# Optimization experiments

Hardware: AMD Instinct MI355X
Metric: run time of the kernel (lower is better)

The kernel has to match this reference:

```python
import jax, jax.numpy as jnp
import numpy as np

N = 8192      # number of tokens (input_dim in the original code)
D = 512       # hidden/embedding dim
R = 20        # number of dependency labels (2R with reverses)
L = 2         # num_layers
OUT = 256     # output_dim


def setup_inputs() -> dict:
    key = jax.random.key(0)
    ks = jax.random.split(key, 10)
    s = 0.02
    return {
        "x": jax.random.normal(ks[0], (N, D), dtype=jnp.float32),
        "dep_idx": jax.random.randint(ks[1], (N,), 0, N, dtype=jnp.int32),
        "rel_idx": jax.random.randint(ks[2], (N,), 0, R, dtype=jnp.int32),
        "gov_idx": jax.random.randint(ks[3], (N,), 0, N, dtype=jnp.int32),
        "W_self": jax.random.normal(ks[4], (L, D, D), dtype=jnp.float32) * s,
        "b_self": jax.random.normal(ks[5], (L, D), dtype=jnp.float32) * s,
        "W_rel": jax.random.normal(ks[6], (L, 2 * R, D, D), dtype=jnp.float32) * s,
        "b_rel": jax.random.normal(ks[7], (L, 2 * R, D), dtype=jnp.float32) * s,
        "W_ff": jax.random.normal(ks[8], (OUT, D), dtype=jnp.float32) * s,
        "b_ff": jax.random.normal(ks[9], (OUT,), dtype=jnp.float32) * s,
    }


def _gcn_layer(x, dep_idx, rel_idx, gov_idx, Ws, bs, Wr, br):
    # self transform applied to every token: temp[idx] = W_self @ x[idx] + b
    out = x @ Ws.T + bs  # [N, D]
    # relation-specific message passing: loop over the small fixed label set.
    # For each relation r: transform ALL nodes once (dense GEMM), then
    # mask-gather-scatter only the edges carrying that relation.
    for r in range(R):
        m = (rel_idx == r)[:, None]                      # [E, 1]
        # forward direction: dependent += W_r @ x[governor] + b_r
        h_f = x @ Wr[r].T + br[r]                        # [N, D]
        out = out.at[dep_idx].add(jnp.where(m, h_f[gov_idx], 0.0))
        # reverse direction: governor += W_{r}_r @ x[dependent] + b
        h_b = x @ Wr[R + r].T + br[R + r]                # [N, D]
        out = out.at[gov_idx].add(jnp.where(m, h_b[dep_idx], 0.0))
    return jax.nn.relu(out)


def reference(x, dep_idx, rel_idx, gov_idx, W_self, b_self, W_rel, b_rel, W_ff, b_ff):
    h = x
    for l in range(L):  # dropout_rate=0.0 -> dropout is identity; last layer has no dropout anyway
        h = _gcn_layer(h, dep_idx, rel_idx, gov_idx, W_self[l], b_self[l], W_rel[l], b_rel[l])
    return h @ W_ff.T + b_ff  # [N, OUT]
```

## Files before the change

### kernel.cpp

```cpp
#include <hip/hip_runtime.h>

#define N_TOK 8192
#define DIM   512
#define NREL  20
#define NGRP  40
#define OUTD  256
#define MAXT  168
#define MAXP  (MAXT*128)

typedef unsigned short u16;
typedef u16    u16x8  __attribute__((ext_vector_type(8)));
typedef __bf16 bf16x8 __attribute__((ext_vector_type(8)));
typedef float  f32x4  __attribute__((ext_vector_type(4)));

__device__ __forceinline__ u16 f2bf(float f) {
  union { float f; unsigned u; } v; v.f = f;
  return (u16)((v.u + 0x7FFFu + ((v.u >> 16) & 1u)) >> 16);
}

__global__ void k_cvt(const float* __restrict__ in, u16* __restrict__ out,
                      int n4, int relu) {
  int stride = gridDim.x * blockDim.x;
  for (int i = blockIdx.x * blockDim.x + threadIdx.x; i < n4; i += stride) {
    float4 v = reinterpret_cast<const float4*>(in)[i];
    if (relu) {
      v.x = fmaxf(v.x, 0.f); v.y = fmaxf(v.y, 0.f);
      v.z = fmaxf(v.z, 0.f); v.w = fmaxf(v.w, 0.f);
    }
    reinterpret_cast<ushort4*>(out)[i] =
        make_ushort4(f2bf(v.x), f2bf(v.y), f2bf(v.z), f2bf(v.w));
  }
}

__global__ void k_hist(const int* __restrict__ rel, int* __restrict__ cnt) {
  int e = blockIdx.x * blockDim.x + threadIdx.x;
  if (e < N_TOK) atomicAdd(&cnt[rel[e]], 1);
}
__global__ void k_scan2(const int* __restrict__ cnt, int* __restrict__ po,
                        int* __restrict__ segtab) {
  if (threadIdx.x == 0) {
    int tile = 0, p = 0;
    for (int s = 0; s < NGRP; ++s) {
      int r = (s < NREL) ? s : s - NREL;
      po[s] = p;
      int nt = (cnt[r] + 127) >> 7;
      for (int i = 0; i < nt; ++i) segtab[tile++] = s;
      p += nt << 7;
    }
    po[NGRP] = p;
    for (; tile < MAXT; ++tile) segtab[tile] = -1;
  }
}
__global__ void k_fill2(const int* __restrict__ rel, const int* __restrict__ dep,
                        const int* __restrict__ gov, const int* __restrict__ po,
                        int* __restrict__ cur, int* __restrict__ msrc,
                        int* __restrict__ mdst) {
  int e = blockIdx.x * blockDim.x + threadIdx.x;
  if (e < N_TOK) {
    int r = rel[e];
    int p = atomicAdd(&cur[r], 1);
    int pf = po[r] + p, pb = po[NREL + r] + p;
    msrc[pf] = gov[e]; mdst[pf] = dep[e];
    msrc[pb] = dep[e]; mdst[pb] = gov[e];
  }
}

template <int KIND>
__global__ __launch_bounds__(256) void k_mm(
    const u16* __restrict__ A, const u16* __restrict__ Wb,
    const float* __restrict__ bias,
    const int* __restrict__ msrc, const int* __restrict__ mdst,
    const int* __restrict__ segtab,
    float* __restrict__ Cf, int Nn)
{
  int seg = 0;
  if (KIND == 1) { seg = segtab[blockIdx.x]; if (seg < 0) return; }
  const int m0 = blockIdx.x * 128, n0 = blockIdx.y * 128;
  const u16* Bsrc = Wb + (KIND == 1 ? (size_t)seg * DIM * DIM : 0);

  __shared__ u16 As[128 * 64];
  __shared__ u16 Bs[128 * 64];

  const int t = threadIdx.x, w = t >> 6, l = t & 63;
  const int wm = (w >> 1) * 64, wn = (w & 1) * 64;
  const int lc = l & 15, h8 = l >> 4;
  const int wch = (t & 7) ^ ((t >> 3) & 7);

  const u16* gApt[4]; const u16* gBpt[4]; bool azero[4];
#pragma unroll
  for (int p = 0; p < 4; ++p) {
    const int row = p * 32 + (t >> 3);
    int arow;
    if (KIND == 1) { arow = msrc[m0 + row]; azero[p] = (arow < 0); if (arow < 0) arow = 0; }
    else { arow = m0 + row; azero[p] = false; }
    gApt[p] = A + (size_t)arow * DIM + (t & 7) * 8;
    gBpt[p] = Bsrc + (size_t)(n0 + row) * DIM + (t & 7) * 8;
  }

  f32x4 acc[4][4] = {};

  for (int k0 = 0; k0 < DIM; k0 += 64) {
#pragma unroll
    for (int p = 0; p < 4; ++p) {
      const int row = p * 32 + (t >> 3);
      u16x8 av = {0, 0, 0, 0, 0, 0, 0, 0};
      if (KIND != 1 || !azero[p]) av = *reinterpret_cast<const u16x8*>(gApt[p] + k0);
      *reinterpret_cast<u16x8*>(&As[row * 64 + wch * 8]) = av;
      u16x8 bw = *reinterpret_cast<const u16x8*>(gBpt[p] + k0);
      *reinterpret_cast<u16x8*>(&Bs[row * 64 + wch * 8]) = bw;
    }
    __syncthreads();
#pragma unroll
    for (int ks = 0; ks < 2; ++ks) {
      const int rc = ks * 4 + h8;
      bf16x8 af[4], bfr[4];
#pragma unroll
      for (int mi = 0; mi < 4; ++mi)
        af[mi] = *reinterpret_cast<const bf16x8*>(&As[(wm + mi * 16 + lc) * 64 + (rc ^ (lc & 7)) * 8]);
#pragma unroll
      for (int ni = 0; ni < 4; ++ni)
        bfr[ni] = *reinterpret_cast<const bf16x8*>(&Bs[(wn + ni * 16 + lc) * 64 + (rc ^ (lc & 7)) * 8]);
#pragma unroll
      for (int mi = 0; mi < 4; ++mi)
#pragma unroll
        for (int ni = 0; ni < 4; ++ni)
          acc[mi][ni] = __builtin_amdgcn_mfma_f32_16x16x32_bf16(af[mi], bfr[ni], acc[mi][ni], 0, 0, 0);
    }
    __syncthreads();
  }

  float bv[4];
  const float* bb = (KIND == 1) ? (bias + (size_t)seg * DIM) : bias;
#pragma unroll
  for (int ni = 0; ni < 4; ++ni) bv[ni] = bb[n0 + wn + ni * 16 + lc];

#pragma unroll
  for (int mi = 0; mi < 4; ++mi)
#pragma unroll
    for (int j = 0; j < 4; ++j) {
      const int rloc = wm + mi * 16 + h8 * 4 + j;
      if (KIND == 1) {
        const int dst = mdst[m0 + rloc];
        if (dst >= 0) {
          float* pout = Cf + (size_t)dst * DIM + n0 + wn + lc;
#pragma unroll
          for (int ni = 0; ni < 4; ++ni)
            unsafeAtomicAdd(pout + ni * 16, acc[mi][ni][j] + bv[ni]);
        }
      } else {
        float* pout = Cf + (size_t)(m0 + rloc) * Nn + n0 + wn + lc;
#pragma unroll
        for (int ni = 0; ni < 4; ++ni)
          pout[ni * 16] = acc[mi][ni][j] + bv[ni];
      }
    }
}

extern "C" void kernel_launch(void* const* d_in, const int* in_sizes, int n_in,
                              void* d_out, int out_size, void* d_ws, size_t ws_size,
                              hipStream_t stream) {
  const float* x      = (const float*)d_in[0];
  const int*   dep    = (const int*)d_in[1];
  const int*   rel    = (const int*)d_in[2];
  const int*   gov    = (const int*)d_in[3];
  const float* W_self = (const float*)d_in[4];
  const float* b_self = (const float*)d_in[5];
  const float* W_rel  = (const float*)d_in[6];
  const float* b_rel  = (const float*)d_in[7];
  const float* W_ff   = (const float*)d_in[8];
  const float* b_ff   = (const float*)d_in[9];
  float* out = (float*)d_out;

  char* ws = (char*)d_ws;
  size_t o = 0;
  auto alloc = [&](size_t bytes) -> void* {
    void* p = ws + o;
    o = (o + bytes + 255) & ~(size_t)255;
    return p;
  };
  u16*   Wrel_bf  = (u16*)alloc((size_t)2 * NGRP * DIM * DIM * 2);
  u16*   Wself_bf = (u16*)alloc((size_t)2 * DIM * DIM * 2);
  u16*   Wff_bf   = (u16*)alloc((size_t)OUTD * DIM * 2);
  u16*   hb0      = (u16*)alloc((size_t)N_TOK * DIM * 2);
  u16*   hb1      = (u16*)alloc((size_t)N_TOK * DIM * 2);
  float* outf     = (float*)alloc((size_t)N_TOK * DIM * 4);
  int*   cnt      = (int*)alloc(NREL * 4);
  int*   po       = (int*)alloc((NGRP + 1) * 4);
  int*   cur      = (int*)alloc(NREL * 4);
  int*   msrc     = (int*)alloc(MAXP * 4);
  int*   mdst     = (int*)alloc(MAXP * 4);
  int*   segtab   = (int*)alloc(MAXT * 4);
  (void)ws_size; (void)in_sizes; (void)n_in; (void)out_size;

  k_cvt<<<2048, 256, 0, stream>>>(W_rel,  Wrel_bf,  2 * NGRP * DIM * DIM / 4, 0);
  k_cvt<<<512,  256, 0, stream>>>(W_self, Wself_bf, 2 * DIM * DIM / 4, 0);
  k_cvt<<<128,  256, 0, stream>>>(W_ff,   Wff_bf,   OUTD * DIM / 4, 0);
  k_cvt<<<2048, 256, 0, stream>>>(x, hb0, N_TOK * DIM / 4, 0);

  hipMemsetAsync(cnt, 0, NREL * 4, stream);
  hipMemsetAsync(cur, 0, NREL * 4, stream);
  hipMemsetAsync(msrc, 0xFF, MAXP * 4, stream);
  hipMemsetAsync(mdst, 0xFF, MAXP * 4, stream);
  k_hist<<<N_TOK / 256, 256, 0, stream>>>(rel, cnt);
  k_scan2<<<1, 64, 0, stream>>>(cnt, po, segtab);
  k_fill2<<<N_TOK / 256, 256, 0, stream>>>(rel, dep, gov, po, cur, msrc, mdst);

  u16* hin = hb0;
  u16* hout = hb1;
  for (int l = 0; l < 2; ++l) {
    k_mm<0><<<dim3(64, 4), 256, 0, stream>>>(
        hin, Wself_bf + (size_t)l * DIM * DIM, b_self + (size_t)l * DIM,
        nullptr, nullptr, nullptr, outf, DIM);
    k_mm<1><<<dim3(MAXT, 4), 256, 0, stream>>>(
        hin, Wrel_bf + (size_t)l * NGRP * DIM * DIM,
        b_rel + (size_t)l * NGRP * DIM, msrc, mdst, segtab, outf, DIM);
    k_cvt<<<2048, 256, 0, stream>>>(outf, hout, N_TOK * DIM / 4, 1);
    u16* tmp = hin; hin = hout; hout = tmp;
  }

  k_mm<0><<<dim3(64, 2), 256, 0, stream>>>(
      hin, Wff_bf, b_ff, nullptr, nullptr, nullptr, out, OUTD);
}
```

Before: 362.6 us.

## Merge self and relation GEMMs into one launch and fuse setup kernels

Combines the four weight/input conversion launches into one multi-segment kernel and replaces the histogram, scan and memset launches with a single-block prep kernel that builds offsets and the tile-to-segment table in shared memory. The self-transform GEMM and the relation scatter GEMM now share one launch with a combined grid. Self tiles also accumulate with atomics into an output buffer that is zeroed by a memset each layer. This cuts launch count and lets self and relation tiles run concurrently, at the cost of an extra memset and atomic writes for the dense part.

New measurement: 371.4 us. 2.4% more time.

```diff
diff --git a/kernel.cpp b/kernel.cpp
--- a/kernel.cpp
+++ b/kernel.cpp
@@ -5,6 +5,7 @@
 #define NREL  20
 #define NGRP  40
 #define OUTD  256
+#define STILE 64
 #define MAXT  168
 #define MAXP  (MAXT*128)
 
@@ -18,39 +19,63 @@
   return (u16)((v.u + 0x7FFFu + ((v.u >> 16) & 1u)) >> 16);
 }
 
-__global__ void k_cvt(const float* __restrict__ in, u16* __restrict__ out,
-                      int n4, int relu) {
-  int stride = gridDim.x * blockDim.x;
+__global__ void k_cvt4(const float* __restrict__ s0, u16* __restrict__ d0, int m0,
+                       const float* __restrict__ s1, u16* __restrict__ d1, int m1,
+                       const float* __restrict__ s2, u16* __restrict__ d2, int m2,
+                       const float* __restrict__ s3, u16* __restrict__ d3, int m3) {
+  const int stride = gridDim.x * blockDim.x;
+  const int t0 = blockIdx.x * blockDim.x + threadIdx.x;
+#define CVT_LOOP(S, D, N)                                                    \
+  for (int i = t0; i < N; i += stride) {                                     \
+    float4 v = reinterpret_cast<const float4*>(S)[i];                        \
+    reinterpret_cast<ushort4*>(D)[i] =                                       \
+        make_ushort4(f2bf(v.x), f2bf(v.y), f2bf(v.z), f2bf(v.w));            \
+  }
+  CVT_LOOP(s0, d0, m0) CVT_LOOP(s1, d1, m1) CVT_LOOP(s2, d2, m2) CVT_LOOP(s3, d3, m3)
+#undef CVT_LOOP
+}
+
+__global__ void k_cvtr(const float* __restrict__ in, u16* __restrict__ out, int n4) {
+  const int stride = gridDim.x * blockDim.x;
   for (int i = blockIdx.x * blockDim.x + threadIdx.x; i < n4; i += stride) {
     float4 v = reinterpret_cast<const float4*>(in)[i];
-    if (relu) {
-      v.x = fmaxf(v.x, 0.f); v.y = fmaxf(v.y, 0.f);
-      v.z = fmaxf(v.z, 0.f); v.w = fmaxf(v.w, 0.f);
-    }
     reinterpret_cast<ushort4*>(out)[i] =
-        make_ushort4(f2bf(v.x), f2bf(v.y), f2bf(v.z), f2bf(v.w));
-  }
-}
-
-__global__ void k_hist(const int* __restrict__ rel, int* __restrict__ cnt) {
-  int e = blockIdx.x * blockDim.x + threadIdx.x;
-  if (e < N_TOK) atomicAdd(&cnt[rel[e]], 1);
-}
-__global__ void k_scan2(const int* __restrict__ cnt, int* __restrict__ po,
-                        int* __restrict__ segtab) {
-  if (threadIdx.x == 0) {
-    int tile = 0, p = 0;
+        make_ushort4(f2bf(fmaxf(v.x, 0.f)), f2bf(fmaxf(v.y, 0.f)),
+                     f2bf(fmaxf(v.z, 0.f)), f2bf(fmaxf(v.w, 0.f)));
+  }
+}
+
+__global__ void k_prep(const int* __restrict__ rel, int* __restrict__ po,
+                       int* __restrict__ segtab, int* __restrict__ cur) {
+  __shared__ int hist[NREL];
+  __shared__ int tpo[NGRP + 1];
+  const int t = threadIdx.x;
+  if (t < NREL) { hist[t] = 0; cur[t] = 0; }
+  __syncthreads();
+  for (int e = t; e < N_TOK; e += 256) atomicAdd(&hist[rel[e]], 1);
+  __syncthreads();
+  if (t == 0) {
+    int acc = 0;
     for (int s = 0; s < NGRP; ++s) {
       int r = (s < NREL) ? s : s - NREL;
-      po[s] = p;
-      int nt = (cnt[r] + 127) >> 7;
-      for (int i = 0; i < nt; ++i) segtab[tile++] = s;
-      p += nt << 7;
-    }
-    po[NGRP] = p;
-    for (; tile < MAXT; ++tile) segtab[tile] = -1;
-  }
-}
+      tpo[s] = acc;
+      acc += (hist[r] + 127) >> 7;
+    }
+    tpo[NGRP] = acc;
+  }
+  __syncthreads();
+  if (t <= NGRP) po[t] = tpo[t] << 7;
+  if (t < MAXT) {
+    int s = -1;
+    if (t < tpo[NGRP]) {
+      int lo = 0, hi = NGRP - 1;
+      while (lo < hi) { int mid = (lo + hi + 1) >> 1; if (tpo[mid] <= t) lo = mid; else hi = mid - 1; }
+      s = lo;
+    }
+    segtab[t] = s;
+  }
+}
+
 __global__ void k_fill2(const int* __restrict__ rel, const int* __restrict__ dep,
                         const int* __restrict__ gov, const int* __restrict__ po,
                         int* __restrict__ cur, int* __restrict__ msrc,
@@ -67,16 +92,28 @@
 
 template <int KIND>
 __global__ __launch_bounds__(256) void k_mm(
-    const u16* __restrict__ A, const u16* __restrict__ Wb,
-    const float* __restrict__ bias,
+    const u16* __restrict__ A,
+    const u16* __restrict__ Wself, const u16* __restrict__ Wrel,
+    const float* __restrict__ bself, const float* __restrict__ brel,
     const int* __restrict__ msrc, const int* __restrict__ mdst,
     const int* __restrict__ segtab,
     float* __restrict__ Cf, int Nn)
 {
-  int seg = 0;
-  if (KIND == 1) { seg = segtab[blockIdx.x]; if (seg < 0) return; }
-  const int m0 = blockIdx.x * 128, n0 = blockIdx.y * 128;
-  const u16* Bsrc = Wb + (KIND == 1 ? (size_t)seg * DIM * DIM : 0);
+  bool isSelf = true;
+  int me0 = 0;
+  const u16* Bsrc = Wself;
+  const float* bb = bself;
+  if (KIND == 2 && blockIdx.x >= STILE) {
+    isSelf = false;
+    const int et = blockIdx.x - STILE;
+    const int seg = segtab[et];
+    if (seg < 0) return;
+    me0 = et * 128;
+    Bsrc = Wrel + (size_t)seg * DIM * DIM;
+    bb = brel + (size_t)seg * DIM;
+  }
+  const int m0 = blockIdx.x * 128;
+  const int n0 = blockIdx.y * 128;
 
   __shared__ u16 As[128 * 64];
   __shared__ u16 Bs[128 * 64];
@@ -91,7 +128,7 @@
   for (int p = 0; p < 4; ++p) {
     const int row = p * 32 + (t >> 3);
     int arow;
-    if (KIND == 1) { arow = msrc[m0 + row]; azero[p] = (arow < 0); if (arow < 0) arow = 0; }
+    if (KIND == 2 && !isSelf) { arow = msrc[me0 + row]; azero[p] = (arow < 0); if (arow < 0) arow = 0; }
     else { arow = m0 + row; azero[p] = false; }
     gApt[p] = A + (size_t)arow * DIM + (t & 7) * 8;
     gBpt[p] = Bsrc + (size_t)(n0 + row) * DIM + (t & 7) * 8;
@@ -104,7 +141,7 @@
     for (int p = 0; p < 4; ++p) {
       const int row = p * 32 + (t >> 3);
       u16x8 av = {0, 0, 0, 0, 0, 0, 0, 0};
-      if (KIND != 1 || !azero[p]) av = *reinterpret_cast<const u16x8*>(gApt[p] + k0);
+      if (!azero[p]) av = *reinterpret_cast<const u16x8*>(gApt[p] + k0);
       *reinterpret_cast<u16x8*>(&As[row * 64 + wch * 8]) = av;
       u16x8 bw = *reinterpret_cast<const u16x8*>(gBpt[p] + k0);
       *reinterpret_cast<u16x8*>(&Bs[row * 64 + wch * 8]) = bw;
@@ -130,7 +167,6 @@
   }
 
   float bv[4];
-  const float* bb = (KIND == 1) ? (bias + (size_t)seg * DIM) : bias;
 #pragma unroll
   for (int ni = 0; ni < 4; ++ni) bv[ni] = bb[n0 + wn + ni * 16 + lc];
 
@@ -139,14 +175,14 @@
 #pragma unroll
     for (int j = 0; j < 4; ++j) {
       const int rloc = wm + mi * 16 + h8 * 4 + j;
-      if (KIND == 1) {
-        const int dst = mdst[m0 + rloc];
-        if (dst >= 0) {
-          float* pout = Cf + (size_t)dst * DIM + n0 + wn + lc;
-#pragma unroll
-          for (int ni = 0; ni < 4; ++ni)
-            unsafeAtomicAdd(pout + ni * 16, acc[mi][ni][j] + bv[ni]);
-        }
+      if (KIND == 2) {
+        int dst;
+        if (isSelf) dst = m0 + rloc;
+        else { dst = mdst[me0 + rloc]; if (dst < 0) continue; }
+        float* pout = Cf + (size_t)dst * DIM + n0 + wn + lc;
+#pragma unroll
+        for (int ni = 0; ni < 4; ++ni)
+          unsafeAtomicAdd(pout + ni * 16, acc[mi][ni][j] + bv[ni]);
       } else {
         float* pout = Cf + (size_t)(m0 + rloc) * Nn + n0 + wn + lc;
 #pragma unroll
@@ -184,7 +220,6 @@
   u16*   hb0      = (u16*)alloc((size_t)N_TOK * DIM * 2);
   u16*   hb1      = (u16*)alloc((size_t)N_TOK * DIM * 2);
   float* outf     = (float*)alloc((size_t)N_TOK * DIM * 4);
-  int*   cnt      = (int*)alloc(NREL * 4);
   int*   po       = (int*)alloc((NGRP + 1) * 4);
   int*   cur      = (int*)alloc(NREL * 4);
   int*   msrc     = (int*)alloc(MAXP * 4);
@@ -192,32 +227,31 @@
   int*   segtab   = (int*)alloc(MAXT * 4);
   (void)ws_size; (void)in_sizes; (void)n_in; (void)out_size;
 
-  k_cvt<<<2048, 256, 0, stream>>>(W_rel,  Wrel_bf,  2 * NGRP * DIM * DIM / 4, 0);
-  k_cvt<<<512,  256, 0, stream>>>(W_self, Wself_bf, 2 * DIM * DIM / 4, 0);
-  k_cvt<<<128,  256, 0, stream>>>(W_ff,   Wff_bf,   OUTD * DIM / 4, 0);
-  k_cvt<<<2048, 256, 0, stream>>>(x, hb0, N_TOK * DIM / 4, 0);
-
-  hipMemsetAsync(cnt, 0, NREL * 4, stream);
-  hipMemsetAsync(cur, 0, NREL * 4, stream);
-  hipMemsetAsync(msrc, 0xFF, MAXP * 4, stream);
-  hipMemsetAsync(mdst, 0xFF, MAXP * 4, stream);
-  k_hist<<<N_TOK / 256, 256, 0, stream>>>(rel, cnt);
-  k_scan2<<<1, 64, 0, stream>>>(cnt, po, segtab);
+  k_cvt4<<<2048, 256, 0, stream>>>(
+      W_rel, Wrel_bf, 2 * NGRP * DIM * DIM / 4,
+      W_self, Wself_bf, 2 * DIM * DIM / 4,
+      W_ff, Wff_bf, OUTD * DIM / 4,
+      x, hb0, N_TOK * DIM / 4);
+
+  hipMemsetAsync(msrc, 0xFF, (size_t)2 * MAXP * 4, stream);
+  k_prep<<<1, 256, 0, stream>>>(rel, po, segtab, cur);
   k_fill2<<<N_TOK / 256, 256, 0, stream>>>(rel, dep, gov, po, cur, msrc, mdst);
 
   u16* hin = hb0;
   u16* hout = hb1;
   for (int l = 0; l < 2; ++l) {
-    k_mm<0><<<dim3(64, 4), 256, 0, stream>>>(
-        hin, Wself_bf + (size_t)l * DIM * DIM, b_self + (size_t)l * DIM,
-        nullptr, nullptr, nullptr, outf, DIM);
-    k_mm<1><<<dim3(MAXT, 4), 256, 0, stream>>>(
-        hin, Wrel_bf + (size_t)l * NGRP * DIM * DIM,
-        b_rel + (size_t)l * NGRP * DIM, msrc, mdst, segtab, outf, DIM);
-    k_cvt<<<2048, 256, 0, stream>>>(outf, hout, N_TOK * DIM / 4, 1);
+    hipMemsetAsync(outf, 0, (size_t)N_TOK * DIM * 4, stream);
+    k_mm<2><<<dim3(STILE + MAXT, DIM / 128), 256, 0, stream>>>(
+        hin,
+        Wself_bf + (size_t)l * DIM * DIM,
+        Wrel_bf + (size_t)l * NGRP * DIM * DIM,
+        b_self + (size_t)l * DIM,
+        b_rel + (size_t)l * NGRP * DIM,
+        msrc, mdst, segtab, outf, DIM);
+    k_cvtr<<<2048, 256, 0, stream>>>(outf, hout, N_TOK * DIM / 4);
     u16* tmp = hin; hin = hout; hout = tmp;
   }
 
-  k_mm<0><<<dim3(64, 2), 256, 0, stream>>>(
-      hin, Wff_bf, b_ff, nullptr, nullptr, nullptr, out, OUTD);
-}
+  k_mm<0><<<dim3(STILE, OUTD / 128), 256, 0, stream>>>(
+      hin, Wff_bf, nullptr, b_ff, nullptr, nullptr, nullptr, nullptr, out, OUTD);
+}
```
